# Kernel tuning notes

Hardware: AMD Instinct MI355X
Metric: run time of the kernel (lower is better)

Reference implementation:

```python
import jax, jax.numpy as jnp
import numpy as np

F_DIM = 128
N_RBF = 20
CUTOFF = 5.0
N_LAYERS = 3
EPS = 1e-8


def setup_inputs() -> dict:
    key = jax.random.key(0)
    ks = jax.random.split(key, 16)
    N, E = 10000, 320000
    atomic_numbers = jax.random.randint(ks[0], (N,), 0, 100)
    r_ij = jax.random.normal(ks[1], (E, 3), dtype=jnp.float32)
    idx_i = jnp.sort(jax.random.randint(ks[2], (E,), 0, N))
    idx_j = jax.random.randint(ks[3], (E,), 0, N)
    emb = jax.random.normal(ks[4], (100, F_DIM), dtype=jnp.float32)
    emb = emb.at[0].set(0.0)  # padding_idx=0
    s = 0.05
    return {
        "atomic_numbers": atomic_numbers,
        "r_ij": r_ij,
        "idx_i": idx_i,
        "idx_j": idx_j,
        "embedding": emb,
        "filt_W": jax.random.normal(ks[5], (N_RBF, N_LAYERS * 3 * F_DIM), dtype=jnp.float32) * s,
        "filt_b": jax.random.normal(ks[6], (N_LAYERS * 3 * F_DIM,), dtype=jnp.float32) * s,
        "int_W1": jax.random.normal(ks[7], (N_LAYERS, F_DIM, F_DIM), dtype=jnp.float32) * s,
        "int_b1": jax.random.normal(ks[8], (N_LAYERS, F_DIM), dtype=jnp.float32) * s,
        "int_W2": jax.random.normal(ks[9], (N_LAYERS, F_DIM, 3 * F_DIM), dtype=jnp.float32) * s,
        "int_b2": jax.random.normal(ks[10], (N_LAYERS, 3 * F_DIM), dtype=jnp.float32) * s,
        "mix_W1": jax.random.normal(ks[11], (N_LAYERS, 2 * F_DIM, F_DIM), dtype=jnp.float32) * s,
        "mix_b1": jax.random.normal(ks[12], (N_LAYERS, F_DIM), dtype=jnp.float32) * s,
        "mix_W2": jax.random.normal(ks[13], (N_LAYERS, F_DIM, 3 * F_DIM), dtype=jnp.float32) * s,
        "mix_b2": jax.random.normal(ks[14], (N_LAYERS, 3 * F_DIM), dtype=jnp.float32) * s,
        "mux_W": jax.random.normal(ks[15], (N_LAYERS, F_DIM, 2 * F_DIM), dtype=jnp.float32) * s,
    }


def _painn(embedding, filt_W, filt_b, int_W1, int_b1, int_W2, int_b2,
           mix_W1, mix_b1, mix_W2, mix_b2, mux_W,
           r_ij, atomic_numbers, idx_i, idx_j):
    N = atomic_numbers.shape[0]
    F = F_DIM
    d_ij = jnp.linalg.norm(r_ij, axis=1, keepdims=True)          # [E,1]
    dir_ij = r_ij / d_ij                                          # [E,3]
    # Gaussian RBF expansion
    offset = jnp.linspace(0.0, CUTOFF, N_RBF, dtype=jnp.float32)
    coeff = -0.5 / (offset[1] - offset[0]) ** 2
    phi = jnp.exp(coeff * (d_ij[..., None] - offset) ** 2)        # [E,1,n_rbf]
    # Cosine cutoff
    fcut = 0.5 * (jnp.cos(d_ij * jnp.pi / CUTOFF) + 1.0) * (d_ij < CUTOFF)  # [E,1]
    filters = (phi @ filt_W + filt_b) * fcut[..., None]           # [E,1,L*3F]
    filter_list = jnp.split(filters, N_LAYERS, axis=-1)

    q = embedding[atomic_numbers][:, None, :]                     # [N,1,F]
    mu = jnp.zeros((N, 3, F), dtype=q.dtype)

    for i in range(N_LAYERS):
        Wij = filter_list[i]                                      # [E,1,3F]
        # interaction
        h = jax.nn.silu(q @ int_W1[i] + int_b1[i])
        x = h @ int_W2[i] + int_b2[i]                             # [N,1,3F]
        xj = x[idx_j]                                             # [E,1,3F]
        muj = mu[idx_j]                                           # [E,3,F]
        xw = Wij * xj
        dq, dmuR, dmumu = jnp.split(xw, 3, axis=-1)               # each [E,1,F]
        dq = jax.ops.segment_sum(dq, idx_i, num_segments=N)       # [N,1,F]
        dmu = dmuR * dir_ij[:, :, None] + dmumu * muj             # [E,3,F]
        dmu = jax.ops.segment_sum(dmu, idx_i, num_segments=N)     # [N,3,F]
        q = q + dq
        mu = mu + dmu
        # mixing
        mu_mix = mu @ mux_W[i]                                    # [N,3,2F]
        mu_V, mu_W = jnp.split(mu_mix, 2, axis=-1)
        mu_Vn = jnp.sqrt(jnp.sum(mu_V ** 2, axis=-2, keepdims=True) + EPS)  # [N,1,F]
        ctx = jnp.concatenate([q, mu_Vn], axis=-1)                # [N,1,2F]
        h = jax.nn.silu(ctx @ mix_W1[i] + mix_b1[i])
        x = h @ mix_W2[i] + mix_b2[i]                             # [N,1,3F]
        dq_i, dmu_i, dqmu_i = jnp.split(x, 3, axis=-1)
        dmu_i = dmu_i * mu_W                                      # [N,3,F]
        dqmu_i = dqmu_i * jnp.sum(mu_V * mu_W, axis=1, keepdims=True)
        q = q + dq_i + dqmu_i
        mu = mu + dmu_i
    return q[:, 0, :], mu


def reference(atomic_numbers, r_ij, idx_i, idx_j, embedding, filt_W, filt_b,
              int_W1, int_b1, int_W2, int_b2, mix_W1, mix_b1, mix_W2, mix_b2, mux_W):
    return _painn(embedding, filt_W, filt_b, int_W1, int_b1, int_W2, int_b2,
                  mix_W1, mix_b1, mix_W2, mix_b2, mux_W,
                  r_ij, atomic_numbers, idx_i, idx_j)
```

## Files before the change

kernel.cpp:

```cpp
#include <hip/hip_runtime.h>
#include <hip/hip_bf16.h>
#include <hip/hip_fp16.h>

#define F_DIM 128
#define N_RBF 20
#define CUTOFF 5.0f
#define PI_F 3.14159265358979323846f
#define NPB 4

typedef float v2f __attribute__((ext_vector_type(2)));
typedef __attribute__((ext_vector_type(8))) short bf16x8;
typedef __attribute__((ext_vector_type(4))) float f32x4;
typedef _Float16 h2f __attribute__((ext_vector_type(2)));
typedef _Float16 f16x8 __attribute__((ext_vector_type(8)));

__device__ __forceinline__ unsigned int bf16_rtne(float f) {
    unsigned int u = __float_as_uint(f);
    u += 0x7fffu + ((u >> 16) & 1u);
    return u >> 16;
}
__device__ __forceinline__ unsigned int pack_bf2(float lo, float hi) {
    return bf16_rtne(lo) | (bf16_rtne(hi) << 16);
}
__device__ __forceinline__ float unpk_lo(unsigned int u) {
    return __uint_as_float(u << 16);
}
__device__ __forceinline__ float unpk_hi(unsigned int u) {
    return __uint_as_float(u & 0xffff0000u);
}
__device__ __forceinline__ float bf16_to_f(unsigned short s) {
    return __uint_as_float(((unsigned int)s) << 16);
}
__device__ __forceinline__ unsigned int pack_h2(float lo, float hi) {
    h2f h = (h2f){(_Float16)lo, (_Float16)hi};
    return __builtin_bit_cast(unsigned int, h);
}
__device__ __forceinline__ unsigned short f16_bits(float f) {
    _Float16 h = (_Float16)f;
    return __builtin_bit_cast(unsigned short, h);
}
__device__ __forceinline__ float f16_to_f(unsigned short s) {
    return (float)__builtin_bit_cast(_Float16, s);
}

__global__ __launch_bounds__(256) void k_rowptr(const int* __restrict__ idx_i,
                                                int* __restrict__ row_ptr, int N, int E) {
    int i = blockIdx.x * blockDim.x + threadIdx.x;
    if (i > N) return;
    if (i == N) { row_ptr[N] = E; return; }
    int lo = 0, hi = E;
    while (lo < hi) {
        int mid = (lo + hi) >> 1;
        if (idx_i[mid] < i) lo = mid + 1; else hi = mid;
    }
    row_ptr[i] = lo;
}

__global__ __launch_bounds__(256) void k_init(const int* __restrict__ Z,
                                              const float* __restrict__ emb,
                                              float* __restrict__ q,
                                              unsigned int* __restrict__ P,
                                              float* __restrict__ muD, int N) {
    int idx = blockIdx.x * blockDim.x + threadIdx.x;
    if (idx < N * F_DIM) {
        int n = idx >> 7, f = idx & 127;
        q[idx] = emb[Z[n] * F_DIM + f];
    }
    if (idx < N * 384) { P[idx] = 0u; muD[idx] = 0.f; }
}

__global__ __launch_bounds__(256) void k_prep(const float* __restrict__ muxW,
                                              const float* __restrict__ W1,
                                              const float* __restrict__ W2,
                                              const float* __restrict__ iW1,
                                              const float* __restrict__ iW2,
                                              const float* __restrict__ filt_W,
                                              const float* __restrict__ filt_b,
                                              unsigned short* __restrict__ muxWt,
                                              unsigned short* __restrict__ W1t,
                                              unsigned short* __restrict__ W2t,
                                              unsigned short* __restrict__ iW1t,
                                              unsigned short* __restrict__ iW2t,
                                              unsigned short* __restrict__ filtWt) {
    int idx = blockIdx.x * 256 + threadIdx.x;
    if (idx < 98304) {
        int l = idx / 32768, rem = idx % 32768;
        int c = rem / 128, k = rem % 128;
        muxWt[idx] = (unsigned short)bf16_rtne(muxW[l * 32768 + k * 256 + c]);
    } else if (idx < 196608) {
        int i2 = idx - 98304;
        int l = i2 / 32768, rem = i2 % 32768;
        int c = rem / 256, k = rem % 256;
        W1t[i2] = (unsigned short)bf16_rtne(W1[l * 32768 + k * 128 + c]);
    } else if (idx < 344064) {
        int i2 = idx - 196608;
        int l = i2 / 49152, rem = i2 % 49152;
        int c = rem / 128, k = rem % 128;
        W2t[i2] = (unsigned short)bf16_rtne(W2[l * 49152 + k * 384 + c]);
    } else if (idx < 393216) {
        int i2 = idx - 344064;
        int l = i2 / 16384, rem = i2 % 16384;
        int c = rem / 128, k = rem % 128;
        iW1t[i2] = (unsigned short)bf16_rtne(iW1[l * 16384 + k * 128 + c]);
    } else if (idx < 540672) {
        int i2 = idx - 393216;
        int l = i2 / 49152, rem = i2 % 49152;
        int c = rem / 128, k = rem % 128;
        iW2t[i2] = (unsigned short)bf16_rtne(iW2[l * 49152 + k * 384 + c]);
    } else if (idx < 568320) {
        int i2 = idx - 540672;
        int l = i2 / 9216, rem = i2 % 9216;
        int c = rem / 24, k = rem % 24;
        float v = 0.f;
        if (k < 20)       v = filt_W[k * 1152 + l * 384 + c];
        else if (k == 20) v = filt_b[l * 384 + c];
        _Float16 hv = (_Float16)v;
        filtWt[i2] = __builtin_bit_cast(unsigned short, hv);
    }
}

__global__ __launch_bounds__(256) void k_geom(const float* __restrict__ r,
                                              unsigned int* __restrict__ geom, int E) {
    int e = blockIdx.x * blockDim.x + threadIdx.x;
    if (e >= E) return;
    float x = r[e * 3], y = r[e * 3 + 1], z = r[e * 3 + 2];
    float d = sqrtf(x * x + y * y + z * z);
    float inv = 1.f / d;
    float fc = (d < CUTOFF) ? 0.5f * (__cosf(d * (PI_F / CUTOFF)) + 1.f) : 0.f;
    unsigned int* g = geom + (size_t)e * 16;
    float dx = x * inv, dy = y * inv, dz = z * inv;
    g[0] = __float_as_uint(dx);
    g[1] = __float_as_uint(dy);
    g[2] = __float_as_uint(dz);
    g[3] = __float_as_uint(fc);
    const float delta = CUTOFF / (N_RBF - 1);
    const float coeff = -0.5f / (delta * delta);
    float ph[N_RBF];
#pragma unroll
    for (int k = 0; k < N_RBF; k++) {
        float t = d - k * delta;
        ph[k] = __expf(coeff * t * t) * fc;
    }
#pragma unroll
    for (int k = 0; k < N_RBF / 2; k++)
        g[4 + k] = pack_h2(ph[2 * k], ph[2 * k + 1]);
    g[14] = pack_h2(fc, dx);
    g[15] = pack_h2(dy, dz);
}

__global__ __launch_bounds__(256) void k_node_mfma(
        const float* __restrict__ q,
        const unsigned short* __restrict__ iW1t,
        const float* __restrict__ b1,
        const unsigned short* __restrict__ iW2t,
        const float* __restrict__ b2,
        unsigned int* __restrict__ P, int N) {
    __shared__ unsigned short A[16 * 136];
    __shared__ unsigned short Ah[16 * 136];
    __shared__ float Xs[16 * 396];
    int t = threadIdx.x;
    int w = t >> 6, l = t & 63, quad = l >> 4, c0 = l & 15;
    int n0 = blockIdx.x * 16;

#pragma unroll
    for (int i = 0; i < 4; i++) {
        int flat = i * 256 + t;
        int node = flat >> 6, cp = flat & 63;
        int gn = n0 + node;
        unsigned int v = 0u;
        if (gn < N) { const float* s = q + (size_t)gn * 128 + 2 * cp; v = pack_bf2(s[0], s[1]); }
        *(unsigned int*)&A[node * 136 + 2 * cp] = v;
    }
    __syncthreads();

    bf16x8 a1[4];
#pragma unroll
    for (int ks = 0; ks < 4; ks++)
        a1[ks] = *(const bf16x8*)&A[c0 * 136 + ks * 32 + quad * 8];
#pragma unroll
    for (int jj = 0; jj < 2; jj++) {
        int jg = 2 * w + jj;
        float bb = b1[16 * jg + c0];
        f32x4 acc = (f32x4){bb, bb, bb, bb};
#pragma unroll
        for (int ks = 0; ks < 4; ks++) {
            bf16x8 b = *(const bf16x8*)&iW1t[(16 * jg + c0) * 128 + ks * 32 + quad * 8];
            acc = __builtin_amdgcn_mfma_f32_16x16x32_bf16(a1[ks], b, acc, 0, 0, 0);
        }
#pragma unroll
        for (int r = 0; r < 4; r++) {
            float aa = acc[r];
            Ah[(quad * 4 + r) * 136 + 16 * jg + c0] =
                (unsigned short)bf16_rtne(aa / (1.f + __expf(-aa)));
        }
    }
    __syncthreads();

    bf16x8 a3[4];
#pragma unroll
    for (int ks = 0; ks < 4; ks++)
        a3[ks] = *(const bf16x8*)&Ah[c0 * 136 + ks * 32 + quad * 8];
#pragma unroll
    for (int jj = 0; jj < 6; jj++) {
        int jx = 6 * w + jj;
        float bb = b2[16 * jx + c0];
        f32x4 acc = (f32x4){bb, bb, bb, bb};
#pragma unroll
        for (int ks = 0; ks < 4; ks++) {
            bf16x8 b = *(const bf16x8*)&iW2t[(16 * jx + c0) * 128 + ks * 32 + quad * 8];
            acc = __builtin_amdgcn_mfma_f32_16x16x32_bf16(a3[ks], b, acc, 0, 0, 0);
        }
#pragma unroll
        for (int r = 0; r < 4; r++)
            Xs[(quad * 4 + r) * 396 + 16 * jx + c0] = acc[r];
    }
    __syncthreads();

    int n = t >> 4, fi = (t & 15) * 8;
    int gn = n0 + n;
    if (gn < N) {
        size_t base = (size_t)gn * 384;
        unsigned int d[8];
#pragma unroll
        for (int k = 0; k < 8; k++) {
            float x0 = Xs[n * 396 + fi + k];
            float x1 = Xs[n * 396 + 128 + fi + k];
            float x2 = Xs[n * 396 + 256 + fi + k];
            d[k] = pack_bf2(x0, x1);
            ((unsigned short*)&P[base + 256 + fi + k])[0] = (unsigned short)bf16_rtne(x2);
        }
        *(uint4*)&P[base + fi]     = make_uint4(d[0], d[1], d[2], d[3]);
        *(uint4*)&P[base + fi + 4] = make_uint4(d[4], d[5], d[6], d[7]);
    }
}

__device__ __forceinline__ f16x8 load_phi_frag(const unsigned int* __restrict__ geom,
                                               int ts, int c0, int quad, int E) {
    int ea = ts + c0;
    if (ea >= E) ea = E - 1;
    f16x8 a = {};
    if (quad < 3)
        a = *(const f16x8*)&geom[(size_t)ea * 16 + 4 + quad * 4];
    return a;
}

template <bool HAS_MU>
__global__ __launch_bounds__(256, 8) void k_edge(
        const unsigned int* __restrict__ P,
        const unsigned int* __restrict__ geom,
        const int* __restrict__ idx_j,
        const int* __restrict__ row_ptr,
        const unsigned short* __restrict__ filtWt,
        float* __restrict__ q,
        float* __restrict__ muD, int N, int E) {
    constexpr int NT = HAS_MU ? 6 : 4;
    constexpr int WS = HAS_MU ? 412 : 268;
    __shared__ unsigned short Ws[16 * WS];
    __shared__ float red[4][128];
    int t = threadIdx.x;
    int f = t & 127;
    int sub = __builtin_amdgcn_readfirstlane(t >> 7);
    int w = t >> 6, l = t & 63, quad = l >> 4, c0 = l & 15;

    f16x8 Bf[NT];
#pragma unroll
    for (int jj = 0; jj < NT; jj++) {
        int jx = NT * w + jj;
        f16x8 b = {};
        if (quad < 3)
            b = *(const f16x8*)&filtWt[(16 * jx + c0) * 24 + quad * 8];
        Bf[jj] = b;
    }

    int i0 = blockIdx.x * NPB;
    for (int nn = 0; nn < NPB; nn++) {
        int i = i0 + nn;
        if (i >= N) break;
        int rs = __builtin_amdgcn_readfirstlane(row_ptr[i]);
        int re = __builtin_amdgcn_readfirstlane(row_ptr[i + 1]);
        float dq = 0.f;
        v2f dm01 = (v2f){0.f, 0.f};
        float dm2 = 0.f;

        f16x8 a = load_phi_frag(geom, rs, c0, quad, E);
        for (int ts = rs; ts < re; ts += 16) {
#pragma unroll
            for (int jj = 0; jj < NT; jj++) {
                int jx = NT * w + jj;
                f32x4 acc = (f32x4){0.f, 0.f, 0.f, 0.f};
                acc = __builtin_amdgcn_mfma_f32_16x16x32_f16(a, Bf[jj], acc, 0, 0, 0);
#pragma unroll
                for (int r = 0; r < 4; r++)
                    Ws[(quad * 4 + r) * WS + 16 * jx + c0] = f16_bits(acc[r]);
            }
            __syncthreads();
            if (ts + 16 < re) a = load_phi_frag(geom, ts + 16, c0, quad, E);

            int te = (re < ts + 16) ? re : ts + 16;
            for (int e = ts + sub; e < te; e += 2) {
                int j = __builtin_amdgcn_readfirstlane(idx_j[e]);
                const unsigned int* Pj = P + (size_t)j * 384;
                unsigned int A = Pj[f];
                unsigned int B = 0, C = 0;
                if (HAS_MU) { B = Pj[128 + f]; C = Pj[256 + f]; }

                const float* g = (const float*)(geom + (size_t)e * 16);
                float dirx = g[0], diry = g[1], dirz = g[2];

                int eloc = e - ts;
                float wq = f16_to_f(Ws[eloc * WS + f]);
                float wr = f16_to_f(Ws[eloc * WS + 128 + f]);

                float xq = unpk_lo(A), xr = unpk_hi(A);
                dq += wq * xq;
                float s_r = wr * xr;
                if (HAS_MU) {
                    float wm = f16_to_f(Ws[eloc * WS + 256 + f]);
                    float xm = unpk_lo(C);
                    float s_m = wm * xm;
                    dm01 += (v2f){s_r, s_r} * (v2f){dirx, diry} +
                            (v2f){s_m, s_m} * (v2f){unpk_lo(B), unpk_hi(B)};
                    dm2  += s_r * dirz + s_m * unpk_hi(C);
                } else {
                    dm01 += (v2f){s_r, s_r} * (v2f){dirx, diry};
                    dm2  += s_r * dirz;
                }
            }
            __syncthreads();
        }

        if (sub == 1) { red[0][f] = dq; red[1][f] = dm01.x; red[2][f] = dm01.y; red[3][f] = dm2; }
        __syncthreads();
        if (sub == 0) {
            dq += red[0][f];
            float d0 = dm01.x + red[1][f], d1 = dm01.y + red[2][f];
            dm2 += red[3][f];
            q[(size_t)i * 128 + f] += dq;
            size_t base = (size_t)i * 384;
            if (HAS_MU) {
                muD[base + f]       += d0;
                muD[base + 128 + f] += d1;
                muD[base + 256 + f] += dm2;
            } else {
                muD[base + f]       = d0;
                muD[base + 128 + f] = d1;
                muD[base + 256 + f] = dm2;
            }
        }
        __syncthreads();
    }
}

__global__ __launch_bounds__(256) void k_mix_fused(
        float* __restrict__ q, float* __restrict__ mu,
        const unsigned short* __restrict__ muxWt,
        const unsigned short* __restrict__ W1t,
        const unsigned short* __restrict__ W2t,
        const float* __restrict__ b1,
        const float* __restrict__ b2,
        const unsigned short* __restrict__ niW1t,
        const float* __restrict__ nib1,
        const unsigned short* __restrict__ niW2t,
        const float* __restrict__ nib2,
        int has_node,
        unsigned int* __restrict__ P, int N) {
    __shared__ unsigned short A[16 * 264];
    __shared__ unsigned short Wsp[3 * 16 * 136];
    __shared__ float Xs[16 * 396];
    __shared__ float Ss[16 * 140];
    int t = threadIdx.x;
    int w = t >> 6, l = t & 63, quad = l >> 4, c0 = l & 15;
    int n0 = blockIdx.x * 16;

#pragma unroll
    for (int i = 0; i < 4; i++) {
        int flat = i * 256 + t;
        int node = flat >> 6, cp = flat & 63;
        int gn = n0 + node;
        unsigned int v = 0u;
        if (gn < N) { const float* s = q + (size_t)gn * 128 + 2 * cp; v = pack_bf2(s[0], s[1]); }
        *(unsigned int*)&A[node * 264 + 2 * cp] = v;
    }

    f32x4 vn2[2], S[2];
#pragma unroll
    for (int jj = 0; jj < 2; jj++) { vn2[jj] = (f32x4){0,0,0,0}; S[jj] = (f32x4){0,0,0,0}; }

    for (int c = 0; c < 3; c++) {
#pragma unroll
        for (int i = 0; i < 4; i++) {
            int flat = i * 256 + t;
            int node = flat >> 6, cp = flat & 63;
            int gn = n0 + node;
            unsigned int v = 0u;
            if (gn < N) {
                const float* s = mu + (size_t)gn * 384 + c * 128 + 2 * cp;
                v = pack_bf2(s[0], s[1]);
            }
            *(unsigned int*)&A[node * 264 + 128 + 2 * cp] = v;
        }
        __syncthreads();
        bf16x8 af[4];
#pragma unroll
        for (int ks = 0; ks < 4; ks++)
            af[ks] = *(const bf16x8*)&A[c0 * 264 + 128 + ks * 32 + quad * 8];
#pragma unroll
        for (int jj = 0; jj < 2; jj++) {
            int jv = 2 * w + jj;
            f32x4 V = (f32x4){0,0,0,0}, Wm = (f32x4){0,0,0,0};
#pragma unroll
            for (int ks = 0; ks < 4; ks++) {
                bf16x8 bV = *(const bf16x8*)&muxWt[(16 * jv + c0) * 128 + ks * 32 + quad * 8];
                V = __builtin_amdgcn_mfma_f32_16x16x32_bf16(af[ks], bV, V, 0, 0, 0);
            }
#pragma unroll
            for (int ks = 0; ks < 4; ks++) {
                bf16x8 bW = *(const bf16x8*)&muxWt[(16 * (jv + 8) + c0) * 128 + ks * 32 + quad * 8];
                Wm = __builtin_amdgcn_mfma_f32_16x16x32_bf16(af[ks], bW, Wm, 0, 0, 0);
            }
            vn2[jj] += V * V;
            S[jj]   += V * Wm;
#pragma unroll
            for (int r = 0; r < 4; r++)
                Wsp[c * 2176 + (quad * 4 + r) * 136 + 16 * jv + c0] =
                    (unsigned short)bf16_rtne(Wm[r]);
        }
        __syncthreads();
    }

#pragma unroll
    for (int jj = 0; jj < 2; jj++) {
        int jv = 2 * w + jj;
#pragma unroll
        for (int r = 0; r < 4; r++)
            A[(quad * 4 + r) * 264 + 128 + 16 * jv + c0] =
                (unsigned short)bf16_rtne(sqrtf(vn2[jj][r] + 1e-8f));
    }
    __syncthreads();

    bf16x8 a2[8];
#pragma unroll
    for (int ks = 0; ks < 8; ks++)
        a2[ks] = *(const bf16x8*)&A[c0 * 264 + ks * 32 + quad * 8];
    {
        unsigned short htmp[2][4];
#pragma unroll
        for (int jj = 0; jj < 2; jj++) {
            int jg = 2 * w + jj;
            float bb = b1[16 * jg + c0];
            f32x4 acc = (f32x4){bb, bb, bb, bb};
#pragma unroll
            for (int ks = 0; ks < 8; ks++) {
                bf16x8 b = *(const bf16x8*)&W1t[(16 * jg + c0) * 256 + ks * 32 + quad * 8];
                acc = __builtin_amdgcn_mfma_f32_16x16x32_bf16(a2[ks], b, acc, 0, 0, 0);
            }
#pragma unroll
            for (int r = 0; r < 4; r++) {
                float aa = acc[r];
                htmp[jj][r] = (unsigned short)bf16_rtne(aa / (1.f + __expf(-aa)));
            }
        }
        __syncthreads();
#pragma unroll
        for (int jj = 0; jj < 2; jj++) {
            int jg = 2 * w + jj;
#pragma unroll
            for (int r = 0; r < 4; r++)
                A[(quad * 4 + r) * 264 + 128 + 16 * jg + c0] = htmp[jj][r];
        }
    }
    __syncthreads();

    bf16x8 a3[4];
#pragma unroll
    for (int ks = 0; ks < 4; ks++)
        a3[ks] = *(const bf16x8*)&A[c0 * 264 + 128 + ks * 32 + quad * 8];
#pragma unroll
    for (int jj = 0; jj < 6; jj++) {
        int jx = 6 * w + jj;
        float bb = b2[16 * jx + c0];
        f32x4 acc = (f32x4){bb, bb, bb, bb};
#pragma unroll
        for (int ks = 0; ks < 4; ks++) {
            bf16x8 b = *(const bf16x8*)&W2t[(16 * jx + c0) * 128 + ks * 32 + quad * 8];
            acc = __builtin_amdgcn_mfma_f32_16x16x32_bf16(a3[ks], b, acc, 0, 0, 0);
        }
#pragma unroll
        for (int r = 0; r < 4; r++)
            Xs[(quad * 4 + r) * 396 + 16 * jx + c0] = acc[r];
    }
#pragma unroll
    for (int jj = 0; jj < 2; jj++) {
        int jv = 2 * w + jj;
#pragma unroll
        for (int r = 0; r < 4; r++)
            Ss[(quad * 4 + r) * 140 + 16 * jv + c0] = S[jj][r];
    }
    __syncthreads();

    int n = t >> 4, fi = (t & 15) * 8;
    int gn = n0 + n;
    if (gn < N) {
        float* qp = q + (size_t)gn * 128 + fi;
        float qn[8];
#pragma unroll
        for (int k = 0; k < 8; k++) {
            qn[k] = qp[k] + Xs[n * 396 + fi + k] +
                    Xs[n * 396 + 256 + fi + k] * Ss[n * 140 + fi + k];
            qp[k] = qn[k];
        }
        unsigned int qd[4];
#pragma unroll
        for (int p = 0; p < 4; p++) qd[p] = pack_bf2(qn[2 * p], qn[2 * p + 1]);
        *(uint4*)&A[n * 264 + fi] = make_uint4(qd[0], qd[1], qd[2], qd[3]);

        size_t base = (size_t)gn * 384;
        float m[3][8];
#pragma unroll
        for (int c = 0; c < 3; c++) {
            float* mp = mu + base + c * 128 + fi;
#pragma unroll
            for (int k = 0; k < 8; k++) {
                m[c][k] = mp[k] + Xs[n * 396 + 128 + fi + k] *
                                  bf16_to_f(Wsp[c * 2176 + n * 136 + fi + k]);
                mp[k] = m[c][k];
            }
        }
        unsigned int d[8];
#pragma unroll
        for (int k = 0; k < 8; k++) {
            d[k] = pack_bf2(m[0][k], m[1][k]);
            ((unsigned short*)&P[base + 256 + fi + k])[1] = (unsigned short)bf16_rtne(m[2][k]);
        }
        *(uint4*)&P[base + 128 + fi]     = make_uint4(d[0], d[1], d[2], d[3]);
        *(uint4*)&P[base + 128 + fi + 4] = make_uint4(d[4], d[5], d[6], d[7]);
    }
    __syncthreads();

    if (has_node) {
        unsigned short* Ah = Wsp;
        bf16x8 a1[4];
#pragma unroll
        for (int ks = 0; ks < 4; ks++)
            a1[ks] = *(const bf16x8*)&A[c0 * 264 + ks * 32 + quad * 8];
#pragma unroll
        for (int jj = 0; jj < 2; jj++) {
            int jg = 2 * w + jj;
            float bb = nib1[16 * jg + c0];
            f32x4 acc = (f32x4){bb, bb, bb, bb};
#pragma unroll
            for (int ks = 0; ks < 4; ks++) {
                bf16x8 b = *(const bf16x8*)&niW1t[(16 * jg + c0) * 128 + ks * 32 + quad * 8];
                acc = __builtin_amdgcn_mfma_f32_16x16x32_bf16(a1[ks], b, acc, 0, 0, 0);
            }
#pragma unroll
            for (int r = 0; r < 4; r++) {
                float aa = acc[r];
                Ah[(quad * 4 + r) * 136 + 16 * jg + c0] =
                    (unsigned short)bf16_rtne(aa / (1.f + __expf(-aa)));
            }
        }
        __syncthreads();

        bf16x8 a4[4];
#pragma unroll
        for (int ks = 0; ks < 4; ks++)
            a4[ks] = *(const bf16x8*)&Ah[c0 * 136 + ks * 32 + quad * 8];
#pragma unroll
        for (int jj = 0; jj < 6; jj++) {
            int jx = 6 * w + jj;
            float bb = nib2[16 * jx + c0];
            f32x4 acc = (f32x4){bb, bb, bb, bb};
#pragma unroll
            for (int ks = 0; ks < 4; ks++) {
                bf16x8 b = *(const bf16x8*)&niW2t[(16 * jx + c0) * 128 + ks * 32 + quad * 8];
                acc = __builtin_amdgcn_mfma_f32_16x16x32_bf16(a4[ks], b, acc, 0, 0, 0);
            }
#pragma unroll
            for (int r = 0; r < 4; r++)
                Xs[(quad * 4 + r) * 396 + 16 * jx + c0] = acc[r];
        }
        __syncthreads();

        if (gn < N) {
            size_t base = (size_t)gn * 384;
            unsigned int d[8];
#pragma unroll
            for (int k = 0; k < 8; k++) {
                float x0 = Xs[n * 396 + fi + k];
                float x1 = Xs[n * 396 + 128 + fi + k];
                float x2 = Xs[n * 396 + 256 + fi + k];
                d[k] = pack_bf2(x0, x1);
                ((unsigned short*)&P[base + 256 + fi + k])[0] = (unsigned short)bf16_rtne(x2);
            }
            *(uint4*)&P[base + fi]     = make_uint4(d[0], d[1], d[2], d[3]);
            *(uint4*)&P[base + fi + 4] = make_uint4(d[4], d[5], d[6], d[7]);
        }
    }
}

extern "C" void kernel_launch(void* const* d_in, const int* in_sizes, int n_in,
                              void* d_out, int out_size, void* d_ws, size_t ws_size,
                              hipStream_t stream) {
    const int*   Z      = (const int*)d_in[0];
    const float* r_ij   = (const float*)d_in[1];
    const int*   idx_i  = (const int*)d_in[2];
    const int*   idx_j  = (const int*)d_in[3];
    const float* emb    = (const float*)d_in[4];
    const float* filt_W = (const float*)d_in[5];
    const float* filt_b = (const float*)d_in[6];
    const float* int_W1 = (const float*)d_in[7];
    const float* int_b1 = (const float*)d_in[8];
    const float* int_W2 = (const float*)d_in[9];
    const float* int_b2 = (const float*)d_in[10];
    const float* mix_W1 = (const float*)d_in[11];
    const float* mix_b1 = (const float*)d_in[12];
    const float* mix_W2 = (const float*)d_in[13];
    const float* mix_b2 = (const float*)d_in[14];
    const float* mux_W  = (const float*)d_in[15];

    int N = in_sizes[0];
    int E = in_sizes[2];

    float* q   = (float*)d_out;
    float* muD = q + (size_t)N * 128;

    unsigned int* geom = (unsigned int*)d_ws;
    unsigned int* P = geom + (size_t)E * 16;
    int* row_ptr = (int*)(P + (size_t)N * 384);
    uintptr_t waddr = (uintptr_t)(row_ptr + N + 1);
    waddr = (waddr + 15) & ~(uintptr_t)15;
    unsigned short* muxWt = (unsigned short*)waddr;
    unsigned short* W1t   = muxWt + 98304;
    unsigned short* W2t   = W1t + 98304;
    unsigned short* iW1t  = W2t + 147456;
    unsigned short* iW2t  = iW1t + 49152;
    unsigned short* filtWt = iW2t + 147456;

    k_rowptr<<<(N + 1 + 255) / 256, 256, 0, stream>>>(idx_i, row_ptr, N, E);
    k_init<<<((size_t)N * 384 + 255) / 256, 256, 0, stream>>>(Z, emb, q, P, muD, N);
    k_geom<<<(E + 255) / 256, 256, 0, stream>>>(r_ij, geom, E);
    k_prep<<<2220, 256, 0, stream>>>(mux_W, mix_W1, mix_W2, int_W1, int_W2, filt_W, filt_b,
                                     muxWt, W1t, W2t, iW1t, iW2t, filtWt);

    int tiles = (N + 15) / 16;
    k_node_mfma<<<tiles, 256, 0, stream>>>(
        q, iW1t, int_b1, iW2t, int_b2, P, N);
    for (int l = 0; l < 3; l++) {
        if (l == 0)
            k_edge<false><<<(N + NPB - 1) / NPB, 256, 0, stream>>>(
                P, geom, idx_j, row_ptr, filtWt, q, muD, N, E);
        else
            k_edge<true><<<(N + NPB - 1) / NPB, 256, 0, stream>>>(
                P, geom, idx_j, row_ptr, filtWt + (size_t)l * 9216, q, muD, N, E);
        int nl = (l < 2) ? (l + 1) : 0;
        k_mix_fused<<<tiles, 256, 0, stream>>>(
            q, muD, muxWt + (size_t)l * 32768, W1t + (size_t)l * 32768,
            W2t + (size_t)l * 49152, mix_b1 + l * 128, mix_b2 + l * 384,
            iW1t + (size_t)nl * 16384, int_b1 + nl * 128,
            iW2t + (size_t)nl * 49152, int_b2 + nl * 384,
            (l < 2) ? 1 : 0, P, N);
    }
}
```

Before: 541.3 us.

## Merge preprocessing kernels, fold embedding lookup into node kernel, prefetch mix loads

Merges the row-pointer, geometry and weight-prep kernels into one launch that dispatches on block index. Drops the init kernel by doing the embedding gather inside the first node kernel, which also writes q, and stops zero-filling P and muD. In the mix kernel it loads the q and all three mu components into registers before the LDS stores and packs the S buffer into the Xs region. It also adds a launch bound asking for three blocks per CU. The main risk is correctness: parts of P, such as the high halves of its third segment, may have relied on the zero-fill.

```diff
diff --git a/kernel.cpp b/kernel.cpp
--- a/kernel.cpp
+++ b/kernel.cpp
@@ -43,46 +43,65 @@
     return (float)__builtin_bit_cast(_Float16, s);
 }
 
-__global__ __launch_bounds__(256) void k_rowptr(const int* __restrict__ idx_i,
-                                                int* __restrict__ row_ptr, int N, int E) {
-    int i = blockIdx.x * blockDim.x + threadIdx.x;
-    if (i > N) return;
-    if (i == N) { row_ptr[N] = E; return; }
-    int lo = 0, hi = E;
-    while (lo < hi) {
-        int mid = (lo + hi) >> 1;
-        if (idx_i[mid] < i) lo = mid + 1; else hi = mid;
-    }
-    row_ptr[i] = lo;
-}
-
-__global__ __launch_bounds__(256) void k_init(const int* __restrict__ Z,
-                                              const float* __restrict__ emb,
-                                              float* __restrict__ q,
-                                              unsigned int* __restrict__ P,
-                                              float* __restrict__ muD, int N) {
-    int idx = blockIdx.x * blockDim.x + threadIdx.x;
-    if (idx < N * F_DIM) {
-        int n = idx >> 7, f = idx & 127;
-        q[idx] = emb[Z[n] * F_DIM + f];
-    }
-    if (idx < N * 384) { P[idx] = 0u; muD[idx] = 0.f; }
-}
-
-__global__ __launch_bounds__(256) void k_prep(const float* __restrict__ muxW,
-                                              const float* __restrict__ W1,
-                                              const float* __restrict__ W2,
-                                              const float* __restrict__ iW1,
-                                              const float* __restrict__ iW2,
-                                              const float* __restrict__ filt_W,
-                                              const float* __restrict__ filt_b,
-                                              unsigned short* __restrict__ muxWt,
-                                              unsigned short* __restrict__ W1t,
-                                              unsigned short* __restrict__ W2t,
-                                              unsigned short* __restrict__ iW1t,
-                                              unsigned short* __restrict__ iW2t,
-                                              unsigned short* __restrict__ filtWt) {
-    int idx = blockIdx.x * 256 + threadIdx.x;
+__global__ __launch_bounds__(256) void k_pre(
+        const int* __restrict__ idx_i, int* __restrict__ row_ptr,
+        const float* __restrict__ r, unsigned int* __restrict__ geom,
+        const float* __restrict__ muxW,
+        const float* __restrict__ W1,
+        const float* __restrict__ W2,
+        const float* __restrict__ iW1,
+        const float* __restrict__ iW2,
+        const float* __restrict__ filt_W,
+        const float* __restrict__ filt_b,
+        unsigned short* __restrict__ muxWt,
+        unsigned short* __restrict__ W1t,
+        unsigned short* __restrict__ W2t,
+        unsigned short* __restrict__ iW1t,
+        unsigned short* __restrict__ iW2t,
+        unsigned short* __restrict__ filtWt,
+        int N, int E, int nbR, int nbG) {
+    int bid = blockIdx.x;
+    if (bid < nbR) {
+        int i = bid * 256 + threadIdx.x;
+        if (i > N) return;
+        if (i == N) { row_ptr[N] = E; return; }
+        int lo = 0, hi = E;
+        while (lo < hi) {
+            int mid = (lo + hi) >> 1;
+            if (idx_i[mid] < i) lo = mid + 1; else hi = mid;
+        }
+        row_ptr[i] = lo;
+        return;
+    }
+    if (bid < nbR + nbG) {
+        int e = (bid - nbR) * 256 + threadIdx.x;
+        if (e >= E) return;
+        float x = r[e * 3], y = r[e * 3 + 1], z = r[e * 3 + 2];
+        float d = sqrtf(x * x + y * y + z * z);
+        float inv = 1.f / d;
+        float fc = (d < CUTOFF) ? 0.5f * (__cosf(d * (PI_F / CUTOFF)) + 1.f) : 0.f;
+        unsigned int* g = geom + (size_t)e * 16;
+        float dx = x * inv, dy = y * inv, dz = z * inv;
+        g[0] = __float_as_uint(dx);
+        g[1] = __float_as_uint(dy);
+        g[2] = __float_as_uint(dz);
+        g[3] = __float_as_uint(fc);
+        const float delta = CUTOFF / (N_RBF - 1);
+        const float coeff = -0.5f / (delta * delta);
+        float ph[N_RBF];
+#pragma unroll
+        for (int k = 0; k < N_RBF; k++) {
+            float t = d - k * delta;
+            ph[k] = __expf(coeff * t * t) * fc;
+        }
+#pragma unroll
+        for (int k = 0; k < N_RBF / 2; k++)
+            g[4 + k] = pack_h2(ph[2 * k], ph[2 * k + 1]);
+        g[14] = pack_h2(fc, dx);
+        g[15] = pack_h2(dy, dz);
+        return;
+    }
+    int idx = (bid - nbR - nbG) * 256 + threadIdx.x;
     if (idx < 98304) {
         int l = idx / 32768, rem = idx % 32768;
         int c = rem / 128, k = rem % 128;
@@ -119,37 +138,10 @@
     }
 }
 
-__global__ __launch_bounds__(256) void k_geom(const float* __restrict__ r,
-                                              unsigned int* __restrict__ geom, int E) {
-    int e = blockIdx.x * blockDim.x + threadIdx.x;
-    if (e >= E) return;
-    float x = r[e * 3], y = r[e * 3 + 1], z = r[e * 3 + 2];
-    float d = sqrtf(x * x + y * y + z * z);
-    float inv = 1.f / d;
-    float fc = (d < CUTOFF) ? 0.5f * (__cosf(d * (PI_F / CUTOFF)) + 1.f) : 0.f;
-    unsigned int* g = geom + (size_t)e * 16;
-    float dx = x * inv, dy = y * inv, dz = z * inv;
-    g[0] = __float_as_uint(dx);
-    g[1] = __float_as_uint(dy);
-    g[2] = __float_as_uint(dz);
-    g[3] = __float_as_uint(fc);
-    const float delta = CUTOFF / (N_RBF - 1);
-    const float coeff = -0.5f / (delta * delta);
-    float ph[N_RBF];
-#pragma unroll
-    for (int k = 0; k < N_RBF; k++) {
-        float t = d - k * delta;
-        ph[k] = __expf(coeff * t * t) * fc;
-    }
-#pragma unroll
-    for (int k = 0; k < N_RBF / 2; k++)
-        g[4 + k] = pack_h2(ph[2 * k], ph[2 * k + 1]);
-    g[14] = pack_h2(fc, dx);
-    g[15] = pack_h2(dy, dz);
-}
-
 __global__ __launch_bounds__(256) void k_node_mfma(
-        const float* __restrict__ q,
+        const int* __restrict__ Z,
+        const float* __restrict__ emb,
+        float* __restrict__ q,
         const unsigned short* __restrict__ iW1t,
         const float* __restrict__ b1,
         const unsigned short* __restrict__ iW2t,
@@ -168,7 +160,13 @@
         int node = flat >> 6, cp = flat & 63;
         int gn = n0 + node;
         unsigned int v = 0u;
-        if (gn < N) { const float* s = q + (size_t)gn * 128 + 2 * cp; v = pack_bf2(s[0], s[1]); }
+        if (gn < N) {
+            const float* s = emb + (size_t)Z[gn] * 128 + 2 * cp;
+            float s0 = s[0], s1 = s[1];
+            v = pack_bf2(s0, s1);
+            float* qo = q + (size_t)gn * 128 + 2 * cp;
+            qo[0] = s0; qo[1] = s1;
+        }
         *(unsigned int*)&A[node * 136 + 2 * cp] = v;
     }
     __syncthreads();
@@ -351,7 +349,7 @@
     }
 }
 
-__global__ __launch_bounds__(256) void k_mix_fused(
+__global__ __launch_bounds__(256, 3) void k_mix_fused(
         float* __restrict__ q, float* __restrict__ mu,
         const unsigned short* __restrict__ muxWt,
         const unsigned short* __restrict__ W1t,
@@ -364,41 +362,56 @@
         const float* __restrict__ nib2,
         int has_node,
         unsigned int* __restrict__ P, int N) {
-    __shared__ unsigned short A[16 * 264];
-    __shared__ unsigned short Wsp[3 * 16 * 136];
-    __shared__ float Xs[16 * 396];
-    __shared__ float Ss[16 * 140];
+    constexpr int XS = 516;
+    __shared__ __align__(16) unsigned char LDSm[16 * 264 * 2 + 3 * 16 * 136 * 2 + 16 * XS * 4];
+    unsigned short* A   = (unsigned short*)LDSm;
+    unsigned short* Wsp = (unsigned short*)(LDSm + 8448);
+    float*          Xs  = (float*)(LDSm + 21504);
+
     int t = threadIdx.x;
     int w = t >> 6, l = t & 63, quad = l >> 4, c0 = l & 15;
     int n0 = blockIdx.x * 16;
 
+    int nodeS[4], cpS[4], gnS[4];
 #pragma unroll
     for (int i = 0; i < 4; i++) {
         int flat = i * 256 + t;
-        int node = flat >> 6, cp = flat & 63;
-        int gn = n0 + node;
+        nodeS[i] = flat >> 6; cpS[i] = flat & 63; gnS[i] = n0 + nodeS[i];
+    }
+    unsigned int vq[4], vmu[3][4];
+#pragma unroll
+    for (int i = 0; i < 4; i++) {
         unsigned int v = 0u;
-        if (gn < N) { const float* s = q + (size_t)gn * 128 + 2 * cp; v = pack_bf2(s[0], s[1]); }
-        *(unsigned int*)&A[node * 264 + 2 * cp] = v;
-    }
+        if (gnS[i] < N) {
+            const float* s = q + (size_t)gnS[i] * 128 + 2 * cpS[i];
+            v = pack_bf2(s[0], s[1]);
+        }
+        vq[i] = v;
+    }
+#pragma unroll
+    for (int c = 0; c < 3; c++)
+#pragma unroll
+        for (int i = 0; i < 4; i++) {
+            unsigned int v = 0u;
+            if (gnS[i] < N) {
+                const float* s = mu + (size_t)gnS[i] * 384 + c * 128 + 2 * cpS[i];
+                v = pack_bf2(s[0], s[1]);
+            }
+            vmu[c][i] = v;
+        }
+#pragma unroll
+    for (int i = 0; i < 4; i++)
+        *(unsigned int*)&A[nodeS[i] * 264 + 2 * cpS[i]] = vq[i];
 
     f32x4 vn2[2], S[2];
 #pragma unroll
     for (int jj = 0; jj < 2; jj++) { vn2[jj] = (f32x4){0,0,0,0}; S[jj] = (f32x4){0,0,0,0}; }
 
+#pragma unroll
     for (int c = 0; c < 3; c++) {
 #pragma unroll
-        for (int i = 0; i < 4; i++) {
-            int flat = i * 256 + t;
-            int node = flat >> 6, cp = flat & 63;
-            int gn = n0 + node;
-            unsigned int v = 0u;
-            if (gn < N) {
-                const float* s = mu + (size_t)gn * 384 + c * 128 + 2 * cp;
-                v = pack_bf2(s[0], s[1]);
-            }
-            *(unsigned int*)&A[node * 264 + 128 + 2 * cp] = v;
-        }
+        for (int i = 0; i < 4; i++)
+            *(unsigned int*)&A[nodeS[i] * 264 + 128 + 2 * cpS[i]] = vmu[c][i];
         __syncthreads();
         bf16x8 af[4];
 #pragma unroll
@@ -487,14 +500,14 @@
         }
 #pragma unroll
         for (int r = 0; r < 4; r++)
-            Xs[(quad * 4 + r) * 396 + 16 * jx + c0] = acc[r];
+            Xs[(quad * 4 + r) * XS + 16 * jx + c0] = acc[r];
     }
 #pragma unroll
     for (int jj = 0; jj < 2; jj++) {
         int jv = 2 * w + jj;
 #pragma unroll
         for (int r = 0; r < 4; r++)
-            Ss[(quad * 4 + r) * 140 + 16 * jv + c0] = S[jj][r];
+            Xs[(quad * 4 + r) * XS + 388 + 16 * jv + c0] = S[jj][r];
     }
     __syncthreads();
 
@@ -505,8 +518,8 @@
         float qn[8];
 #pragma unroll
         for (int k = 0; k < 8; k++) {
-            qn[k] = qp[k] + Xs[n * 396 + fi + k] +
-                    Xs[n * 396 + 256 + fi + k] * Ss[n * 140 + fi + k];
+            qn[k] = qp[k] + Xs[n * XS + fi + k] +
+                    Xs[n * XS + 256 + fi + k] * Xs[n * XS + 388 + fi + k];
             qp[k] = qn[k];
         }
         unsigned int qd[4];
@@ -521,7 +534,7 @@
             float* mp = mu + base + c * 128 + fi;
 #pragma unroll
             for (int k = 0; k < 8; k++) {
-                m[c][k] = mp[k] + Xs[n * 396 + 128 + fi + k] *
+                m[c][k] = mp[k] + Xs[n * XS + 128 + fi + k] *
                                   bf16_to_f(Wsp[c * 2176 + n * 136 + fi + k]);
                 mp[k] = m[c][k];
             }
@@ -578,7 +591,7 @@
             }
 #pragma unroll
             for (int r = 0; r < 4; r++)
-                Xs[(quad * 4 + r) * 396 + 16 * jx + c0] = acc[r];
+                Xs[(quad * 4 + r) * XS + 16 * jx + c0] = acc[r];
         }
         __syncthreads();
 
@@ -587,9 +600,9 @@
             unsigned int d[8];
 #pragma unroll
             for (int k = 0; k < 8; k++) {
-                float x0 = Xs[n * 396 + fi + k];
-                float x1 = Xs[n * 396 + 128 + fi + k];
-                float x2 = Xs[n * 396 + 256 + fi + k];
+                float x0 = Xs[n * XS + fi + k];
+                float x1 = Xs[n * XS + 128 + fi + k];
+                float x2 = Xs[n * XS + 256 + fi + k];
                 d[k] = pack_bf2(x0, x1);
                 ((unsigned short*)&P[base + 256 + fi + k])[0] = (unsigned short)bf16_rtne(x2);
             }
@@ -637,15 +650,16 @@
     unsigned short* iW2t  = iW1t + 49152;
     unsigned short* filtWt = iW2t + 147456;
 
-    k_rowptr<<<(N + 1 + 255) / 256, 256, 0, stream>>>(idx_i, row_ptr, N, E);
-    k_init<<<((size_t)N * 384 + 255) / 256, 256, 0, stream>>>(Z, emb, q, P, muD, N);
-    k_geom<<<(E + 255) / 256, 256, 0, stream>>>(r_ij, geom, E);
-    k_prep<<<2220, 256, 0, stream>>>(mux_W, mix_W1, mix_W2, int_W1, int_W2, filt_W, filt_b,
-                                     muxWt, W1t, W2t, iW1t, iW2t, filtWt);
+    int nbR = (N + 1 + 255) / 256;
+    int nbG = (E + 255) / 256;
+    k_pre<<<nbR + nbG + 2220, 256, 0, stream>>>(
+        idx_i, row_ptr, r_ij, geom,
+        mux_W, mix_W1, mix_W2, int_W1, int_W2, filt_W, filt_b,
+        muxWt, W1t, W2t, iW1t, iW2t, filtWt, N, E, nbR, nbG);
 
     int tiles = (N + 15) / 16;
     k_node_mfma<<<tiles, 256, 0, stream>>>(
-        q, iW1t, int_b1, iW2t, int_b2, P, N);
+        Z, emb, q, iW1t, int_b1, iW2t, int_b2, P, N);
     for (int l = 0; l < 3; l++) {
         if (l == 0)
             k_edge<false><<<(N + NPB - 1) / NPB, 256, 0, stream>>>(
```

Measured after the change: 538.4 us. About the same (-0.5%).
